# Optimization experiments

Measured on AMD Instinct MI355X. Metric: run time of the kernel, lower is better.

## Reference

```python
import jax, jax.numpy as jnp
import numpy as np

N_HEADS = 16
HEAD_DIM = 64
IMG = (32, 32)  # (H, W); s = H*W = 1024


def _split_heads(x, n):
    # (b, 1, s, n*d) -> (b*n, s, d)
    b, _, s, nd = x.shape
    d = nd // n
    return x.reshape(b, s, n, d).transpose(0, 2, 1, 3).reshape(b * n, s, d)


def _merge_heads(x, n):
    # (b*n, s, d) -> (b, 1, s, n*d)
    bn, s, d = x.shape
    b = bn // n
    return x.reshape(b, n, s, d).transpose(0, 2, 1, 3).reshape(b, 1, s, n * d)


def _get_rel_pos(size, rel_pos):
    # q_size == k_size == size, table already has 2*size-1 rows -> no interp
    coords = jnp.arange(size)[:, None] - jnp.arange(size)[None, :] + (size - 1)
    return rel_pos[coords]  # (size, size, d)


def setup_inputs() -> dict:
    key = jax.random.key(0)
    ks = jax.random.split(key, 5)
    b, s, nd = 4, IMG[0] * IMG[1], N_HEADS * HEAD_DIM
    return {
        "q": jax.random.normal(ks[0], (b, 1, s, nd), dtype=jnp.float32),
        "k": jax.random.normal(ks[1], (b, 1, s, nd), dtype=jnp.float32),
        "v": jax.random.normal(ks[2], (b, 1, s, nd), dtype=jnp.float32),
        "rel_pos_h": jax.random.normal(ks[3], (2 * IMG[0] - 1, HEAD_DIM), dtype=jnp.float32),
        "rel_pos_w": jax.random.normal(ks[4], (2 * IMG[1] - 1, HEAD_DIM), dtype=jnp.float32),
    }


def reference(q, k, v, rel_pos_h, rel_pos_w):
    H, W = IMG
    q_, k_, v_ = (_split_heads(x, N_HEADS) for x in (q, k, v))  # (B, s, d), B = b*n
    B, s, d = q_.shape
    scale = d ** (-0.5)
    sim = jnp.einsum('bqd,bkd->bqk', q_, k_) * scale  # (B, s, s)

    Rh = _get_rel_pos(H, rel_pos_h)  # (H, H, d)
    Rw = _get_rel_pos(W, rel_pos_w)  # (W, W, d)
    r_q = q_.reshape(B, H, W, d)
    rel_h = jnp.einsum('bhwc,hkc->bhwk', r_q, Rh)  # (B, H, W, kH)
    rel_w = jnp.einsum('bhwc,wkc->bhwk', r_q, Rw)  # (B, H, W, kW)

    sim = (sim.reshape(B, H, W, H, W)
           + rel_h[:, :, :, :, None]
           + rel_w[:, :, :, None, :]).reshape(B, s, s)

    attn = jax.nn.softmax(sim, axis=-1)
    out = jnp.einsum('bqk,bkd->bqd', attn, v_)
    return _merge_heads(out, N_HEADS)  # (b, 1, s, n*d)
```

## Files before the change

### kernel.cpp

```cpp
#include <hip/hip_runtime.h>
#include <stdint.h>


#define SCALE2 0.18033688f
#define LOG2E  1.44269504f

typedef float  f32x4  __attribute__((ext_vector_type(4)));
typedef __bf16 bf16x8 __attribute__((ext_vector_type(8)));
typedef __bf16 bf16x4 __attribute__((ext_vector_type(4)));

#define AS1 __attribute__((address_space(1)))
#define AS3 __attribute__((address_space(3)))

__device__ inline bf16x8 pack8(f32x4 a, f32x4 b) {
    bf16x8 t;
    t[0]=(__bf16)a.x; t[1]=(__bf16)a.y; t[2]=(__bf16)a.z; t[3]=(__bf16)a.w;
    t[4]=(__bf16)b.x; t[5]=(__bf16)b.y; t[6]=(__bf16)b.z; t[7]=(__bf16)b.w;
    return t;
}

__global__ __launch_bounds__(256) void repack(
        const float* __restrict__ kg, const float* __restrict__ vg,
        char* __restrict__ kp, char* __restrict__ vp) {
    __shared__ float Vt[64 * 68];
    const int t   = threadIdx.x;
    const int idx = blockIdx.x;
    const int bh  = idx >> 4, kt = idx & 15;
    const int bb  = bh >> 4, nh = bh & 15;
    const int inbase = bb * 1048576 + nh * 64;
    char* kout = kp + bh * 131072 + kt * 8192;
    char* vout = vp + bh * 131072 + kt * 8192;

    const int r  = t >> 2;
    const int c0 = (t & 3) << 4;

    {
        const float* src = kg + inbase + (kt * 64 + r) * 1024 + c0;
        f32x4 a = ((const f32x4*)src)[0], b = ((const f32x4*)src)[1];
        f32x4 c = ((const f32x4*)src)[2], d = ((const f32x4*)src)[3];
        const int swz = (r & 7) << 4;
        *(bf16x8*)(kout + r * 128 + ((c0 * 2) ^ swz))      = pack8(a, b);
        *(bf16x8*)(kout + r * 128 + ((c0 * 2 + 16) ^ swz)) = pack8(c, d);
    }
    {
        const float* src = vg + inbase + (kt * 64 + r) * 1024 + c0;
        f32x4 a = ((const f32x4*)src)[0], b = ((const f32x4*)src)[1];
        f32x4 c = ((const f32x4*)src)[2], d = ((const f32x4*)src)[3];
        float* dst = &Vt[r * 68 + c0];
        ((f32x4*)dst)[0] = a; ((f32x4*)dst)[1] = b;
        ((f32x4*)dst)[2] = c; ((f32x4*)dst)[3] = d;
    }
    __syncthreads();
    {
        const int d0  = r;
        const int kk0 = c0;
        float x[16];
#pragma unroll
        for (int j = 0; j < 16; ++j) x[j] = Vt[(kk0 + j) * 68 + d0];
        f32x4 a = {x[0], x[1], x[2], x[3]},   b = {x[4], x[5], x[6], x[7]};
        f32x4 c = {x[8], x[9], x[10], x[11]}, d = {x[12], x[13], x[14], x[15]};
        const int swz = (d0 & 7) << 4;
        *(bf16x8*)(vout + d0 * 128 + ((kk0 * 2) ^ swz))      = pack8(a, b);
        *(bf16x8*)(vout + d0 * 128 + ((kk0 * 2 + 16) ^ swz)) = pack8(c, d);
    }
}

__global__ __launch_bounds__(256, 4) void attn(
        const float* __restrict__ qg,
        const char* __restrict__ kp, const char* __restrict__ vp,
        const float* __restrict__ rph, const float* __restrict__ rpw,
        float* __restrict__ outg) {
    __shared__ float ThS[64 * 32];
    __shared__ __align__(16) char arena[32768];
    float* Ql  = (float*)arena;
    float* TwS = (float*)(arena + 17408);

    const int tid  = threadIdx.x;
    const int w    = tid >> 6, lane = tid & 63;
    const int quad = lane >> 4, n16 = lane & 15;
    const int sw16 = (n16 & 7) << 4;

    const int idx = blockIdx.x;
    const int xc  = idx & 7;
    const int r_  = idx >> 3;
    const int hp  = r_ & 15;
    const int bh  = xc + ((r_ >> 4) << 3);

    const int bb = bh >> 4, nh = bh & 15;
    const int h0 = hp << 1;
    const int base = bb * 1048576 + nh * 64;
    const int sq0  = h0 * 32;
    const char* kpb = kp + bh * 131072;
    const char* vpb = vp + bh * 131072;

    {
        int r0 = tid >> 4, c0 = (tid & 15) << 2;
#pragma unroll
        for (int k = 0; k < 4; ++k) {
            int row = k * 16 + r0;
            f32x4 v = *(const f32x4*)(qg + base + (sq0 + row) * 1024 + c0);
            *(f32x4*)&Ql[row * 68 + c0] = v;
        }
    }
    __syncthreads();

    {
        const int wu = __builtin_amdgcn_readfirstlane(w);
        const float* qrow = &Ql[lane * 68];
        const float* hb = rph + h0 * 64;
        const float* wb = rpw - 33 * 64;
        float acc[24];
#pragma unroll
        for (int i = 0; i < 24; ++i) acc[i] = 0.f;
        for (int cq = 0; cq < 16; ++cq) {
            f32x4 qv = *(const f32x4*)(qrow + cq * 4);
#pragma unroll
            for (int i = 0; i < 24; ++i) {
                int cid = wu * 24 + i;
                const float* tb = (cid < 33 ? hb : wb) + cid * 64;
                f32x4 tv = *(const f32x4*)(tb + cq * 4);
                acc[i] += qv.x * tv.x + qv.y * tv.y + qv.z * tv.z + qv.w * tv.w;
            }
        }
#pragma unroll
        for (int i = 0; i < 24; ++i) {
            int cid = wu * 24 + i;
            float v = acc[i] * LOG2E;
            if (cid < 33) {
                int kh = (lane >> 5) + 31 - cid;
                if (kh >= 0 && kh < 32)
                    *(float*)((char*)ThS + lane * 128 + ((kh * 4) ^ ((lane & 7) << 4))) = v;
            } else {
                int kw = (lane & 31) + 31 - (cid - 33);
                if (kw >= 0 && kw < 32)
                    TwS[lane * 36 + kw] = v;
            }
        }
    }

    const int qn = w * 16 + n16;
    bf16x8 qf[2];
#pragma unroll
    for (int ch = 0; ch < 2; ++ch) {
        const float* qp = &Ql[qn * 68 + ch * 32 + quad * 8];
        f32x4 a = ((const f32x4*)qp)[0];
        f32x4 b = ((const f32x4*)qp)[1];
        qf[ch] = pack8(a, b);
    }
    __syncthreads();

    float rwm2[2][4];
    {
        float mh = -1e30f, mw = -1e30f;
#pragma unroll
        for (int i = 0; i < 8; ++i) {
            f32x4 a = *(const f32x4*)((const char*)ThS + qn * 128 + ((i * 16) ^ sw16));
            f32x4 b = *(const f32x4*)&TwS[qn * 36 + i * 4];
            mh = fmaxf(mh, fmaxf(fmaxf(a.x, a.y), fmaxf(a.z, a.w)));
            mw = fmaxf(mw, fmaxf(fmaxf(b.x, b.y), fmaxf(b.z, b.w)));
        }
        float M = mh + mw;
#pragma unroll
        for (int g = 0; g < 2; ++g)
#pragma unroll
            for (int r = 0; r < 4; ++r)
                rwm2[g][r] = TwS[qn * 36 + g * 16 + quad * 4 + r] - M;
    }

    float lr = 0.f;
    f32x4 oc[4];
#pragma unroll
    for (int i = 0; i < 4; ++i) oc[i] = (f32x4){0.f, 0.f, 0.f, 0.f};

    const int lo16 = lane * 16;
    auto GLDS = [&](int buf, int kt) {
        const char* ks = kpb + kt * 8192 + w * 2048 + lo16;
        const char* vs = vpb + kt * 8192 + w * 2048 + lo16;
        char* ld = arena + buf * 16384 + w * 2048;
        __builtin_amdgcn_global_load_lds((const AS1 void*)ks,
                                         (AS3 void*)ld,          16, 0, 0);
        __builtin_amdgcn_global_load_lds((const AS1 void*)(ks + 1024),
                                         (AS3 void*)(ld + 1024), 16, 0, 0);
        __builtin_amdgcn_global_load_lds((const AS1 void*)vs,
                                         (AS3 void*)(ld + 8192), 16, 0, 0);
        __builtin_amdgcn_global_load_lds((const AS1 void*)(vs + 1024),
                                         (AS3 void*)(ld + 9216), 16, 0, 0);
    };

    GLDS(0, 0);

    for (int kt = 0; kt < 16; ++kt) {
        asm volatile("s_waitcnt vmcnt(0) lgkmcnt(0)" ::: "memory");
        __builtin_amdgcn_s_barrier();

        if (kt < 15) GLDS((kt + 1) & 1, kt + 1);

        const char* kbase = arena + (kt & 1) * 16384;
        const char* vbase = kbase + 8192;

        f32x4 s[4];
#pragma unroll
        for (int g = 0; g < 4; ++g) s[g] = (f32x4){0.f, 0.f, 0.f, 0.f};
#pragma unroll
        for (int ch = 0; ch < 2; ++ch)
#pragma unroll
            for (int g = 0; g < 4; ++g) {
                bf16x8 kf = *(const bf16x8*)(kbase + (g * 16 + n16) * 128
                                             + ((ch * 64 + quad * 16) ^ sw16));
                s[g] = __builtin_amdgcn_mfma_f32_16x16x32_bf16(kf, qf[ch], s[g], 0, 0, 0);
            }

        float2 rhp = *(const float2*)((const char*)ThS + qn * 128 + ((kt * 8) ^ sw16));
        float p[4][4];
#pragma unroll
        for (int g = 0; g < 4; ++g) {
            const float rbase = (g >= 2) ? rhp.y : rhp.x;
#pragma unroll
            for (int r = 0; r < 4; ++r)
                p[g][r] = __builtin_amdgcn_exp2f(fmaf(s[g][r], SCALE2, rbase + rwm2[g & 1][r]));
        }
#pragma unroll
        for (int g = 0; g < 4; ++g)
            lr += ((p[g][0] + p[g][1]) + (p[g][2] + p[g][3]));

        bf16x8 pf[2];
#pragma unroll
        for (int ko = 0; ko < 2; ++ko) {
            bf16x8 t;
            t[0] = (__bf16)p[2 * ko][0];     t[1] = (__bf16)p[2 * ko][1];
            t[2] = (__bf16)p[2 * ko][2];     t[3] = (__bf16)p[2 * ko][3];
            t[4] = (__bf16)p[2 * ko + 1][0]; t[5] = (__bf16)p[2 * ko + 1][1];
            t[6] = (__bf16)p[2 * ko + 1][2]; t[7] = (__bf16)p[2 * ko + 1][3];
            pf[ko] = t;
        }

#pragma unroll
        for (int ko = 0; ko < 2; ++ko)
#pragma unroll
            for (int cn = 0; cn < 4; ++cn) {
                const char* vb = vbase + (cn * 16 + n16) * 128;
                bf16x4 a = *(const bf16x4*)(vb + ((ko * 64 + quad * 8) ^ sw16));
                bf16x4 b = *(const bf16x4*)(vb + ((ko * 64 + quad * 8 + 32) ^ sw16));
                bf16x8 vf;
                vf[0] = a[0]; vf[1] = a[1]; vf[2] = a[2]; vf[3] = a[3];
                vf[4] = b[0]; vf[5] = b[1]; vf[6] = b[2]; vf[7] = b[3];
                oc[cn] = __builtin_amdgcn_mfma_f32_16x16x32_bf16(pf[ko], vf, oc[cn], 0, 0, 0);
            }
    }

    lr += __shfl_xor(lr, 16);
    lr += __shfl_xor(lr, 32);
    float linv[4];
#pragma unroll
    for (int r = 0; r < 4; ++r)
        linv[r] = 1.f / __shfl(lr, quad * 4 + r, 64);

#pragma unroll
    for (int r = 0; r < 4; ++r) {
        int ob = base + (sq0 + w * 16 + quad * 4 + r) * 1024 + n16;
        outg[ob]      = oc[0][r] * linv[r];
        outg[ob + 16] = oc[1][r] * linv[r];
        outg[ob + 32] = oc[2][r] * linv[r];
        outg[ob + 48] = oc[3][r] * linv[r];
    }
}

extern "C" void kernel_launch(void* const* d_in, const int* in_sizes, int n_in,
                              void* d_out, int out_size, void* d_ws, size_t ws_size,
                              hipStream_t stream) {
    (void)in_sizes; (void)n_in; (void)out_size; (void)ws_size;
    const float* q   = (const float*)d_in[0];
    const float* k   = (const float*)d_in[1];
    const float* v   = (const float*)d_in[2];
    const float* rph = (const float*)d_in[3];
    const float* rpw = (const float*)d_in[4];
    char* kp = (char*)d_ws;
    char* vp = kp + 8388608;
    repack<<<dim3(1024), 256, 0, stream>>>(k, v, kp, vp);
    attn<<<dim3(1024), 256, 0, stream>>>(q, kp, vp, rph, rpw, (float*)d_out);
}
```

Baseline: 146.5 us.

## Split Q/rel-pos prep into separate kernel and stream V fragments directly to registers

Moves the Q bf16 packing and relative-position bias computation into a new prep kernel that writes per-block results to workspace, so the attention kernel uses less LDS and can run at higher occupancy (launch bound 6). V is repacked into MFMA-fragment order and loaded straight into registers with double-buffered register prefetch, and only K goes through LDS. The cost is an extra kernel launch, a workspace round-trip, and more register pressure from the vA/vB buffers.

```diff
diff --git a/kernel.cpp b/kernel.cpp
--- a/kernel.cpp
+++ b/kernel.cpp
@@ -7,7 +7,6 @@
 
 typedef float  f32x4  __attribute__((ext_vector_type(4)));
 typedef __bf16 bf16x8 __attribute__((ext_vector_type(8)));
-typedef __bf16 bf16x4 __attribute__((ext_vector_type(4)));
 
 #define AS1 __attribute__((address_space(1)))
 #define AS3 __attribute__((address_space(3)))
@@ -52,28 +51,29 @@
     }
     __syncthreads();
     {
-        const int d0  = r;
-        const int kk0 = c0;
-        float x[16];
-#pragma unroll
-        for (int j = 0; j < 16; ++j) x[j] = Vt[(kk0 + j) * 68 + d0];
-        f32x4 a = {x[0], x[1], x[2], x[3]},   b = {x[4], x[5], x[6], x[7]};
-        f32x4 c = {x[8], x[9], x[10], x[11]}, d = {x[12], x[13], x[14], x[15]};
-        const int swz = (d0 & 7) << 4;
-        *(bf16x8*)(vout + d0 * 128 + ((kk0 * 2) ^ swz))      = pack8(a, b);
-        *(bf16x8*)(vout + d0 * 128 + ((kk0 * 2 + 16) ^ swz)) = pack8(c, d);
-    }
-}
-
-__global__ __launch_bounds__(256, 4) void attn(
+        const int wv = t >> 6, l = t & 63;
+        const int n16v = l & 15, quadv = l >> 4;
+#pragma unroll
+        for (int i = 0; i < 2; ++i) {
+            int chunk = wv * 2 + i, ko = chunk >> 2, cn = chunk & 3;
+            int dim = cn * 16 + n16v;
+            float x[8];
+#pragma unroll
+            for (int j = 0; j < 8; ++j)
+                x[j] = Vt[((2 * ko + (j >> 2)) * 16 + quadv * 4 + (j & 3)) * 68 + dim];
+            f32x4 a = {x[0], x[1], x[2], x[3]}, b = {x[4], x[5], x[6], x[7]};
+            *(bf16x8*)(vout + chunk * 1024 + l * 16) = pack8(a, b);
+        }
+    }
+}
+
+__global__ __launch_bounds__(256) void prep(
         const float* __restrict__ qg,
-        const char* __restrict__ kp, const char* __restrict__ vp,
         const float* __restrict__ rph, const float* __restrict__ rpw,
-        float* __restrict__ outg) {
+        char* __restrict__ pz) {
     __shared__ float ThS[64 * 32];
-    __shared__ __align__(16) char arena[32768];
-    float* Ql  = (float*)arena;
-    float* TwS = (float*)(arena + 17408);
+    __shared__ float Ql[64 * 68];
+    __shared__ float TwS[64 * 36];
 
     const int tid  = threadIdx.x;
     const int w    = tid >> 6, lane = tid & 63;
@@ -85,13 +85,10 @@
     const int r_  = idx >> 3;
     const int hp  = r_ & 15;
     const int bh  = xc + ((r_ >> 4) << 3);
-
     const int bb = bh >> 4, nh = bh & 15;
     const int h0 = hp << 1;
     const int base = bb * 1048576 + nh * 64;
     const int sq0  = h0 * 32;
-    const char* kpb = kp + bh * 131072;
-    const char* vpb = vp + bh * 131072;
 
     {
         int r0 = tid >> 4, c0 = (tid & 15) << 2;
@@ -139,13 +136,12 @@
     }
 
     const int qn = w * 16 + n16;
-    bf16x8 qf[2];
-#pragma unroll
-    for (int ch = 0; ch < 2; ++ch) {
-        const float* qp = &Ql[qn * 68 + ch * 32 + quad * 8];
-        f32x4 a = ((const f32x4*)qp)[0];
-        f32x4 b = ((const f32x4*)qp)[1];
-        qf[ch] = pack8(a, b);
+    bf16x8 qf0, qf1;
+    {
+        const float* qp0 = &Ql[qn * 68 + quad * 8];
+        const float* qp1 = &Ql[qn * 68 + 32 + quad * 8];
+        qf0 = pack8(((const f32x4*)qp0)[0], ((const f32x4*)qp0)[1]);
+        qf1 = pack8(((const f32x4*)qp1)[0], ((const f32x4*)qp1)[1]);
     }
     __syncthreads();
 
@@ -167,86 +163,130 @@
                 rwm2[g][r] = TwS[qn * 36 + g * 16 + quad * 4 + r] - M;
     }
 
+    char* wsb = pz + idx * 24576;
+    *(f32x4*)(wsb + (size_t)tid * 32)      = ((const f32x4*)((const char*)ThS + tid * 32))[0];
+    *(f32x4*)(wsb + (size_t)tid * 32 + 16) = ((const f32x4*)((const char*)ThS + tid * 32))[1];
+    f32x4 rv0 = {rwm2[0][0], rwm2[0][1], rwm2[0][2], rwm2[0][3]};
+    f32x4 rv1 = {rwm2[1][0], rwm2[1][1], rwm2[1][2], rwm2[1][3]};
+    *(f32x4*)(wsb + 8192 + (size_t)tid * 32)      = rv0;
+    *(f32x4*)(wsb + 8192 + (size_t)tid * 32 + 16) = rv1;
+    *(bf16x8*)(wsb + 16384 + (size_t)tid * 32)      = qf0;
+    *(bf16x8*)(wsb + 16384 + (size_t)tid * 32 + 16) = qf1;
+}
+
+__global__ __launch_bounds__(256, 6) void attn(
+        const char* __restrict__ kp, const char* __restrict__ vp,
+        const char* __restrict__ pz, float* __restrict__ outg) {
+    __shared__ __align__(16) char ThSb[8192];
+    __shared__ __align__(16) char arena[16384];
+
+    const int tid  = threadIdx.x;
+    const int w    = tid >> 6, lane = tid & 63;
+    const int quad = lane >> 4, n16 = lane & 15;
+    const int sw16 = (n16 & 7) << 4;
+
+    const int idx = blockIdx.x;
+    const int xc  = idx & 7;
+    const int r_  = idx >> 3;
+    const int hp  = r_ & 15;
+    const int bh  = xc + ((r_ >> 4) << 3);
+    const int bb = bh >> 4, nh = bh & 15;
+    const int base = bb * 1048576 + nh * 64;
+    const int sq0  = (hp << 1) * 32;
+
+    const char* kpb = kp + bh * 131072;
+    const char* vpb = vp + bh * 131072;
+    const char* wsb = pz + idx * 24576;
+
+    __builtin_amdgcn_global_load_lds((const AS1 void*)(wsb + w * 2048 + lane * 16),
+                                     (AS3 void*)(ThSb + w * 2048), 16, 0, 0);
+    __builtin_amdgcn_global_load_lds((const AS1 void*)(wsb + w * 2048 + 1024 + lane * 16),
+                                     (AS3 void*)(ThSb + w * 2048 + 1024), 16, 0, 0);
+    __builtin_amdgcn_global_load_lds((const AS1 void*)(kpb + w * 2048 + lane * 16),
+                                     (AS3 void*)(arena + w * 2048), 16, 0, 0);
+    __builtin_amdgcn_global_load_lds((const AS1 void*)(kpb + w * 2048 + 1024 + lane * 16),
+                                     (AS3 void*)(arena + w * 2048 + 1024), 16, 0, 0);
+
+    f32x4 rv0 = *(const f32x4*)(wsb + 8192 + tid * 32);
+    f32x4 rv1 = *(const f32x4*)(wsb + 8192 + tid * 32 + 16);
+    bf16x8 qf0 = *(const bf16x8*)(wsb + 16384 + tid * 32);
+    bf16x8 qf1 = *(const bf16x8*)(wsb + 16384 + tid * 32 + 16);
+
+    bf16x8 vA[8], vB[8];
+#pragma unroll
+    for (int c = 0; c < 8; ++c)
+        vA[c] = *(const bf16x8*)(vpb + c * 1024 + lane * 16);
+
+    const int qn = w * 16 + n16;
     float lr = 0.f;
     f32x4 oc[4];
 #pragma unroll
     for (int i = 0; i < 4; ++i) oc[i] = (f32x4){0.f, 0.f, 0.f, 0.f};
 
-    const int lo16 = lane * 16;
-    auto GLDS = [&](int buf, int kt) {
-        const char* ks = kpb + kt * 8192 + w * 2048 + lo16;
-        const char* vs = vpb + kt * 8192 + w * 2048 + lo16;
-        char* ld = arena + buf * 16384 + w * 2048;
-        __builtin_amdgcn_global_load_lds((const AS1 void*)ks,
-                                         (AS3 void*)ld,          16, 0, 0);
-        __builtin_amdgcn_global_load_lds((const AS1 void*)(ks + 1024),
-                                         (AS3 void*)(ld + 1024), 16, 0, 0);
-        __builtin_amdgcn_global_load_lds((const AS1 void*)vs,
-                                         (AS3 void*)(ld + 8192), 16, 0, 0);
-        __builtin_amdgcn_global_load_lds((const AS1 void*)(vs + 1024),
-                                         (AS3 void*)(ld + 9216), 16, 0, 0);
-    };
-
-    GLDS(0, 0);
-
-    for (int kt = 0; kt < 16; ++kt) {
-        asm volatile("s_waitcnt vmcnt(0) lgkmcnt(0)" ::: "memory");
-        __builtin_amdgcn_s_barrier();
-
-        if (kt < 15) GLDS((kt + 1) & 1, kt + 1);
-
-        const char* kbase = arena + (kt & 1) * 16384;
-        const char* vbase = kbase + 8192;
-
-        f32x4 s[4];
-#pragma unroll
-        for (int g = 0; g < 4; ++g) s[g] = (f32x4){0.f, 0.f, 0.f, 0.f};
-#pragma unroll
-        for (int ch = 0; ch < 2; ++ch)
-#pragma unroll
-            for (int g = 0; g < 4; ++g) {
-                bf16x8 kf = *(const bf16x8*)(kbase + (g * 16 + n16) * 128
-                                             + ((ch * 64 + quad * 16) ^ sw16));
-                s[g] = __builtin_amdgcn_mfma_f32_16x16x32_bf16(kf, qf[ch], s[g], 0, 0, 0);
-            }
-
-        float2 rhp = *(const float2*)((const char*)ThS + qn * 128 + ((kt * 8) ^ sw16));
-        float p[4][4];
-#pragma unroll
-        for (int g = 0; g < 4; ++g) {
-            const float rbase = (g >= 2) ? rhp.y : rhp.x;
-#pragma unroll
-            for (int r = 0; r < 4; ++r)
-                p[g][r] = __builtin_amdgcn_exp2f(fmaf(s[g][r], SCALE2, rbase + rwm2[g & 1][r]));
-        }
-#pragma unroll
-        for (int g = 0; g < 4; ++g)
-            lr += ((p[g][0] + p[g][1]) + (p[g][2] + p[g][3]));
-
-        bf16x8 pf[2];
-#pragma unroll
-        for (int ko = 0; ko < 2; ++ko) {
-            bf16x8 t;
-            t[0] = (__bf16)p[2 * ko][0];     t[1] = (__bf16)p[2 * ko][1];
-            t[2] = (__bf16)p[2 * ko][2];     t[3] = (__bf16)p[2 * ko][3];
-            t[4] = (__bf16)p[2 * ko + 1][0]; t[5] = (__bf16)p[2 * ko + 1][1];
-            t[6] = (__bf16)p[2 * ko + 1][2]; t[7] = (__bf16)p[2 * ko + 1][3];
-            pf[ko] = t;
-        }
-
-#pragma unroll
-        for (int ko = 0; ko < 2; ++ko)
-#pragma unroll
-            for (int cn = 0; cn < 4; ++cn) {
-                const char* vb = vbase + (cn * 16 + n16) * 128;
-                bf16x4 a = *(const bf16x4*)(vb + ((ko * 64 + quad * 8) ^ sw16));
-                bf16x4 b = *(const bf16x4*)(vb + ((ko * 64 + quad * 8 + 32) ^ sw16));
-                bf16x8 vf;
-                vf[0] = a[0]; vf[1] = a[1]; vf[2] = a[2]; vf[3] = a[3];
-                vf[4] = b[0]; vf[5] = b[1]; vf[6] = b[2]; vf[7] = b[3];
-                oc[cn] = __builtin_amdgcn_mfma_f32_16x16x32_bf16(pf[ko], vf, oc[cn], 0, 0, 0);
-            }
-    }
+#define BODY(KT, VC, VN) do {                                                     \
+    asm volatile("s_waitcnt vmcnt(0)" ::: "memory");                              \
+    __builtin_amdgcn_s_barrier();                                                 \
+    if ((KT) + 1 < 16) {                                                          \
+        const char* kn_ = kpb + ((KT) + 1) * 8192;                                \
+        char* kd_ = arena + ((((KT) + 1) & 1) * 8192);                            \
+        __builtin_amdgcn_global_load_lds((const AS1 void*)(kn_ + w * 2048 + lane * 16),          \
+                                         (AS3 void*)(kd_ + w * 2048), 16, 0, 0);                 \
+        __builtin_amdgcn_global_load_lds((const AS1 void*)(kn_ + w * 2048 + 1024 + lane * 16),   \
+                                         (AS3 void*)(kd_ + w * 2048 + 1024), 16, 0, 0);          \
+        const char* vn_ = vpb + ((KT) + 1) * 8192 + lane * 16;                    \
+        _Pragma("unroll")                                                         \
+        for (int c_ = 0; c_ < 8; ++c_) VN[c_] = *(const bf16x8*)(vn_ + c_ * 1024);\
+    }                                                                             \
+    const char* kbase_ = arena + (((KT) & 1) * 8192);                             \
+    f32x4 s_[4];                                                                  \
+    _Pragma("unroll")                                                             \
+    for (int g_ = 0; g_ < 4; ++g_) s_[g_] = (f32x4){0.f, 0.f, 0.f, 0.f};          \
+    _Pragma("unroll")                                                             \
+    for (int ch_ = 0; ch_ < 2; ++ch_)                                             \
+        _Pragma("unroll")                                                         \
+        for (int g_ = 0; g_ < 4; ++g_) {                                          \
+            bf16x8 kf_ = *(const bf16x8*)(kbase_ + (g_ * 16 + n16) * 128          \
+                                          + ((ch_ * 64 + quad * 16) ^ sw16));     \
+            s_[g_] = __builtin_amdgcn_mfma_f32_16x16x32_bf16(kf_, ch_ ? qf1 : qf0,\
+                                                             s_[g_], 0, 0, 0);    \
+        }                                                                         \
+    float2 rhp_ = *(const float2*)(ThSb + qn * 128 + (((KT) * 8) ^ sw16));        \
+    float p_[4][4];                                                               \
+    _Pragma("unroll")                                                             \
+    for (int g_ = 0; g_ < 4; ++g_) {                                              \
+        const float rb_ = (g_ >= 2) ? rhp_.y : rhp_.x;                            \
+        const f32x4 rw_ = (g_ & 1) ? rv1 : rv0;                                   \
+        _Pragma("unroll")                                                         \
+        for (int r_2 = 0; r_2 < 4; ++r_2)                                         \
+            p_[g_][r_2] = __builtin_amdgcn_exp2f(fmaf(s_[g_][r_2], SCALE2,        \
+                                                      rb_ + rw_[r_2]));           \
+    }                                                                             \
+    _Pragma("unroll")                                                             \
+    for (int g_ = 0; g_ < 4; ++g_)                                                \
+        lr += ((p_[g_][0] + p_[g_][1]) + (p_[g_][2] + p_[g_][3]));                \
+    bf16x8 pf_[2];                                                                \
+    _Pragma("unroll")                                                             \
+    for (int ko_ = 0; ko_ < 2; ++ko_) {                                           \
+        bf16x8 t_;                                                                \
+        t_[0] = (__bf16)p_[2 * ko_][0];     t_[1] = (__bf16)p_[2 * ko_][1];       \
+        t_[2] = (__bf16)p_[2 * ko_][2];     t_[3] = (__bf16)p_[2 * ko_][3];       \
+        t_[4] = (__bf16)p_[2 * ko_ + 1][0]; t_[5] = (__bf16)p_[2 * ko_ + 1][1];   \
+        t_[6] = (__bf16)p_[2 * ko_ + 1][2]; t_[7] = (__bf16)p_[2 * ko_ + 1][3];   \
+        pf_[ko_] = t_;                                                            \
+    }                                                                             \
+    _Pragma("unroll")                                                             \
+    for (int ko_ = 0; ko_ < 2; ++ko_)                                             \
+        _Pragma("unroll")                                                         \
+        for (int cn_ = 0; cn_ < 4; ++cn_)                                         \
+            oc[cn_] = __builtin_amdgcn_mfma_f32_16x16x32_bf16(pf_[ko_],           \
+                          VC[ko_ * 4 + cn_], oc[cn_], 0, 0, 0);                   \
+} while (0)
+
+    for (int kt = 0; kt < 16; kt += 2) {
+        BODY(kt, vA, vB);
+        BODY(kt + 1, vB, vA);
+    }
+#undef BODY
 
     lr += __shfl_xor(lr, 16);
     lr += __shfl_xor(lr, 32);
@@ -276,6 +316,8 @@
     const float* rpw = (const float*)d_in[4];
     char* kp = (char*)d_ws;
     char* vp = kp + 8388608;
+    char* pz = vp + 8388608;
     repack<<<dim3(1024), 256, 0, stream>>>(k, v, kp, vp);
-    attn<<<dim3(1024), 256, 0, stream>>>(q, kp, vp, rph, rpw, (float*)d_out);
-}
+    prep  <<<dim3(1024), 256, 0, stream>>>(q, rph, rpw, pz);
+    attn  <<<dim3(1024), 256, 0, stream>>>(kp, vp, pz, (float*)d_out);
+}
```

After: 291.6 us. +99.1%, slower.
